# Optimization experiments

Hardware: AMD Instinct MI355X
Metric: run time of the kernel (lower is better)

The kernel has to match this reference:

```python
import jax, jax.numpy as jnp
import numpy as np

LAMBDA = 0.7
RATIO = 3
EPS = 1e-6


def setup_inputs() -> dict:
    key = jax.random.key(0)
    k1, k2, k3 = jax.random.split(key, 3)
    bs, n, w, h = 8, 7, 640, 640
    preds = jax.random.normal(k1, (bs, n, w, h), dtype=jnp.float32)
    labels = jax.random.randint(k2, (bs, n, w, h), 0, 2, dtype=jnp.int32)
    training_mask = jax.random.randint(k3, (bs, w, h), 0, 2, dtype=jnp.int32)
    return {"preds": preds, "labels": labels, "training_mask": training_mask}


def _dice(S, G):
    # S, G: [C, P]; per-channel dice coefficient, then mean over channels
    num = 2.0 * jnp.sum(S * G, axis=-1)
    den = jnp.sum(S * S, axis=-1) + jnp.sum(G * G, axis=-1) + EPS
    return jnp.mean(num / den)


def _single_sample(pred, label, mask):
    # pred, label: [n, P]; mask: [P]
    P = pred.shape[-1]
    p = jax.nn.sigmoid(pred)
    pred_n = p[-1] * mask            # masked full-text prediction
    label_n = label[-1] * mask

    # --- OHEM mask M (cal_M): keep all positives + top (ratio*n_pos) hardest negatives ---
    pos = pred_n >= 0.5
    n_pos = jnp.sum(pos)
    n_neg_all = jnp.sum(~pos)
    k = n_pos * RATIO
    # sigmoid outputs are in (0,1); sentinel -1 pushes positives to the end of the descending sort
    neg_vals = jnp.where(pos, -1.0, pred_n)
    sorted_desc = -jnp.sort(-neg_vals)
    thr = sorted_desc[jnp.clip(k - 1, 0, P - 1)]  # k-th largest negative score
    ohem_active = (n_neg_all > k) & (k > 0)
    M = jnp.where(ohem_active, (pred_n >= thr).astype(jnp.float32), 1.0)

    # L_c: dice loss on OHEM-selected full-text map
    L_c = 1.0 - _dice((pred_n * M)[None, :], (label_n * M)[None, :])

    # L_s: dice loss on shrunk kernels, gated by predicted text region W
    W = (pred_n >= 0.5).astype(jnp.float32)
    L_s = 1.0 - _dice(p[:-1] * W, label[:-1] * W)

    loss = LAMBDA * L_c + (1.0 - LAMBDA) * L_s
    return L_c, L_s, loss


def reference(preds, labels, training_mask):
    bs, n, w, h = preds.shape
    preds = preds.reshape(bs, n, w * h)
    labels = labels.reshape(bs, n, w * h).astype(jnp.float32)
    mask = training_mask.reshape(bs, w * h).astype(jnp.float32)
    L_c, L_s, loss = jax.vmap(_single_sample)(preds, labels, mask)
    # reduction='mean'
    return L_c.mean(), L_s.mean(), loss.mean()
```

## Files before the change

### kernel.cpp

```cpp
#include <hip/hip_runtime.h>

#define BS   8
#define NCH  7
#define PX   409600
#define NBIN 65536
#define NCHK 256
#define EPSF 1e-6f
#define NT   256
#define BPB  200

__device__ __forceinline__ float sigf(float x) {
    return 1.0f / (1.0f + __expf(-x));
}

__device__ __forceinline__ unsigned wred_u(unsigned v) {
    #pragma unroll
    for (int o = 32; o; o >>= 1) v += __shfl_down(v, o);
    return v;
}

__device__ __forceinline__ float wred_f(float v) {
    #pragma unroll
    for (int o = 32; o; o >>= 1) v += __shfl_down(v, o);
    return v;
}

__device__ void select2(const unsigned* __restrict__ chunks,
                        const unsigned* __restrict__ bins,
                        unsigned k, unsigned* out_bin, unsigned* out_rank) {
    __shared__ unsigned cs[256];
    int t = threadIdx.x;
    cs[t] = chunks[t];
    __syncthreads();
    #pragma unroll
    for (int off = 1; off < 256; off <<= 1) {
        unsigned v = cs[t];
        unsigned a = (t + off < 256) ? cs[t + off] : 0u;
        __syncthreads();
        cs[t] = v + a;
        __syncthreads();
    }
    {
        unsigned sfx  = cs[t];
        unsigned sfx1 = (t < 255) ? cs[t + 1] : 0u;
        if (sfx >= k && sfx1 < k) { *out_bin = (unsigned)t; *out_rank = k - sfx1; }
    }
    __syncthreads();
    unsigned chunk = *out_bin, krem = *out_rank;
    cs[t] = bins[chunk * 256 + t];
    __syncthreads();
    #pragma unroll
    for (int off = 1; off < 256; off <<= 1) {
        unsigned v = cs[t];
        unsigned a = (t + off < 256) ? cs[t + off] : 0u;
        __syncthreads();
        cs[t] = v + a;
        __syncthreads();
    }
    {
        unsigned sfx  = cs[t];
        unsigned sfx1 = (t < 255) ? cs[t + 1] : 0u;
        if (sfx >= krem && sfx1 < krem) {
            *out_bin  = chunk * 256 + (unsigned)t;
            *out_rank = krem - sfx1;
        }
    }
    __syncthreads();
}

__global__ __launch_bounds__(256) void k_main(
        const float* __restrict__ preds, const int* __restrict__ labels,
        const int* __restrict__ mask,
        float* __restrict__ psum,
        unsigned* __restrict__ ppos,
        unsigned* __restrict__ pzero,
        unsigned* __restrict__ done) {
    const int tid = threadIdx.x;
    const int b = blockIdx.y, cb = blockIdx.x;
    if (b == 0 && cb == 0 && tid == 0) *done = 0u;

    const float* pr = preds + (size_t)b * NCH * PX;
    const int*   lb = labels + (size_t)b * NCH * PX;
    const int*   mk = mask + (size_t)b * PX;

    float acc[21];
    #pragma unroll
    for (int j = 0; j < 21; j++) acc[j] = 0.f;
    unsigned cnt = 0;

    #pragma unroll
    for (int it = 0; it < 2; ++it) {
        const int g  = cb * NT + tid + it * (BPB * NT);
        const int px = g * 4;
        float4 p6 = *(const float4*)(pr + 6 * PX + px);
        int4   m4 = *(const int4*)(mk + px);
        int4   l6 = *(const int4*)(lb + 6 * PX + px);
        float4 pc[6];
        int4   lc[6];
        #pragma unroll
        for (int c = 0; c < 6; c++) pc[c] = *(const float4*)(pr + c * PX + px);
        #pragma unroll
        for (int c = 0; c < 6; c++) lc[c] = *(const int4*)(lb + c * PX + px);

        float mm[4]  = {(float)m4.x, (float)m4.y, (float)m4.z, (float)m4.w};
        float p6a[4] = {p6.x, p6.y, p6.z, p6.w};
        float l6a[4] = {(float)l6.x, (float)l6.y, (float)l6.z, (float)l6.w};
        float pn[4], W[4];
        #pragma unroll
        for (int u = 0; u < 4; u++) {
            pn[u] = sigf(p6a[u]) * mm[u];
            bool pos = (pn[u] >= 0.5f);
            W[u] = pos ? 1.0f : 0.0f;
            cnt += pos ? 1u : (__float_as_uint(pn[u]) == 0u ? 0x10000u : 0u);
        }
        #pragma unroll
        for (int c = 0; c < 6; c++) {
            float pcs[4] = {pc[c].x, pc[c].y, pc[c].z, pc[c].w};
            float lcs[4] = {(float)lc[c].x, (float)lc[c].y,
                            (float)lc[c].z, (float)lc[c].w};
            #pragma unroll
            for (int u = 0; u < 4; u++) {
                float s = sigf(pcs[u]);
                float l = lcs[u];
                acc[c]      += s * l * W[u];
                acc[6 + c]  += s * s * W[u];
                acc[12 + c] += l * W[u];
            }
        }
        #pragma unroll
        for (int u = 0; u < 4; u++) {
            float ln = l6a[u] * mm[u];
            acc[18] += pn[u] * ln;
            acc[19] += pn[u] * pn[u];
            acc[20] += ln;
        }
    }

    __shared__ float    red[4][21];
    __shared__ unsigned cred[4];
    int lane = tid & 63, wid = tid >> 6;
    #pragma unroll
    for (int j = 0; j < 21; j++) {
        float v = wred_f(acc[j]);
        if (lane == 0) red[wid][j] = v;
    }
    unsigned cv = wred_u(cnt);
    if (lane == 0) cred[wid] = cv;
    __syncthreads();
    if (tid < 21) {
        float tot = red[0][tid] + red[1][tid] + red[2][tid] + red[3][tid];
        psum[((size_t)b * 21 + tid) * BPB + cb] = tot;
    }
    if (tid == 21) {
        unsigned ct = cred[0] + cred[1] + cred[2] + cred[3];
        ppos[b * BPB + cb]  = ct & 0xFFFFu;
        pzero[b * BPB + cb] = ct >> 16;
    }
}

__global__ __launch_bounds__(256) void k_sel(
        const float* __restrict__ preds, const int* __restrict__ labels,
        const int* __restrict__ mask,
        const float* __restrict__ psum, const unsigned* __restrict__ ppos,
        const unsigned* __restrict__ pzero,
        unsigned* __restrict__ histws, unsigned* __restrict__ chunkws,
        float* __restrict__ lcls,
        unsigned* __restrict__ done, float* __restrict__ out) {
    const int tid = threadIdx.x;
    const int b = blockIdx.x;
    int lane = tid & 63, wid = tid >> 6;

    __shared__ unsigned uR[4][2];
    unsigned npv = (tid < BPB) ? ppos[b * BPB + tid] : 0u;
    unsigned zcv = (tid < BPB) ? pzero[b * BPB + tid] : 0u;
    unsigned r0 = wred_u(npv), r1 = wred_u(zcv);
    if (lane == 0) { uR[wid][0] = r0; uR[wid][1] = r1; }
    __syncthreads();
    const unsigned np = uR[0][0] + uR[1][0] + uR[2][0] + uR[3][0];
    const unsigned zc = uR[0][1] + uR[1][1] + uR[2][1] + uR[3][1];

    __shared__ float S[21];
    if (tid < 21) S[tid] = 0.f;
    __syncthreads();
    for (int i = tid; i < 21 * BPB; i += NT) {
        atomicAdd(&S[i / BPB], psum[(size_t)b * 21 * BPB + i]);
    }
    __syncthreads();

    const unsigned k = np * 3u;
    const bool active = ((unsigned)PX - np > k) && (k > 0u);
    const unsigned nzneg = (unsigned)PX - np - zc;

    float Lc_b;
    if (!active || k >= nzneg) {
        Lc_b = 1.0f - 2.0f * S[18] / (S[19] + S[20] + EPSF);
    } else {
        unsigned* h1 = histws + (size_t)b * NBIN;
        unsigned* c1 = chunkws + (size_t)b * NCHK;
        const float* pr6 = preds + ((size_t)b * NCH + 6) * PX;
        const int*   lb6 = labels + ((size_t)b * NCH + 6) * PX;
        const int*   mk  = mask + (size_t)b * PX;

        for (int j = tid; j < NBIN; j += NT) h1[j] = 0u;
        for (int j = tid; j < NCHK; j += NT) c1[j] = 0u;
        __syncthreads();
        for (int gg = tid; gg < PX; gg += NT) {
            float pnx = sigf(pr6[gg]) * (float)mk[gg];
            if (pnx < 0.5f) {
                unsigned bits = __float_as_uint(pnx);
                if (bits) {
                    atomicAdd(&h1[bits >> 16], 1u);
                    atomicAdd(&c1[bits >> 24], 1u);
                }
            }
        }
        __syncthreads();
        if (tid == 0) { atomicAdd(&h1[0], zc); atomicAdd(&c1[0], zc); }
        __syncthreads();

        __shared__ unsigned rb, rr, rb2, rr2;
        select2(c1, h1, k, &rb, &rr);
        float thrv;
        if (rb == 0u) {
            thrv = 0.0f;
        } else {
            unsigned hi = rb;
            for (int j = tid; j < NBIN; j += NT) h1[j] = 0u;
            for (int j = tid; j < NCHK; j += NT) c1[j] = 0u;
            __syncthreads();
            for (int gg = tid; gg < PX; gg += NT) {
                float pnx = sigf(pr6[gg]) * (float)mk[gg];
                if (pnx < 0.5f) {
                    unsigned bits = __float_as_uint(pnx);
                    if (bits && (bits >> 16) == hi) {
                        unsigned lo = bits & 0xFFFFu;
                        atomicAdd(&h1[lo], 1u);
                        atomicAdd(&c1[lo >> 8], 1u);
                    }
                }
            }
            __syncthreads();
            select2(c1, h1, rr, &rb2, &rr2);
            thrv = __uint_as_float((hi << 16) | rb2);
        }
        float a0 = 0.f, a1 = 0.f, a2 = 0.f;
        for (int gg = tid; gg < PX; gg += NT) {
            float m   = (float)mk[gg];
            float pnx = sigf(pr6[gg]) * m;
            if (pnx >= thrv) {
                float ln = (float)lb6[gg] * m;
                a0 += pnx * ln;
                a1 += pnx * pnx;
                a2 += ln;
            }
        }
        __shared__ float aR[4][3];
        float v0 = wred_f(a0), v1 = wred_f(a1), v2 = wred_f(a2);
        if (lane == 0) { aR[wid][0] = v0; aR[wid][1] = v1; aR[wid][2] = v2; }
        __syncthreads();
        float A0 = aR[0][0] + aR[1][0] + aR[2][0] + aR[3][0];
        float A1 = aR[0][1] + aR[1][1] + aR[2][1] + aR[3][1];
        float A2 = aR[0][2] + aR[1][2] + aR[2][2] + aR[3][2];
        Lc_b = 1.0f - 2.0f * A0 / (A1 + A2 + EPSF);
    }

    float ls_acc = 0.f;
    #pragma unroll
    for (int c = 0; c < 6; c++)
        ls_acc += (2.0f * S[c]) / (S[6 + c] + S[12 + c] + EPSF);
    float Ls_b = 1.0f - ls_acc * (1.0f / 6.0f);

    if (tid == 0) {
        lcls[b * 2]     = Lc_b;
        lcls[b * 2 + 1] = Ls_b;
    }

    __shared__ unsigned tick;
    if (tid == 0) {
        __threadfence();
        tick = atomicAdd(done, 1u);
    }
    __syncthreads();
    if (tick != (unsigned)(BS - 1)) return;
    __threadfence();

    float Lc = 0.f, Ls = 0.f;
    if (tid < BS) { Lc = lcls[tid * 2]; Ls = lcls[tid * 2 + 1]; }
    #pragma unroll
    for (int o = 4; o; o >>= 1) { Lc += __shfl_down(Lc, o); Ls += __shfl_down(Ls, o); }
    if (tid == 0) {
        float lc_m = Lc * (1.0f / (float)BS);
        float ls_m = Ls * (1.0f / (float)BS);
        out[0] = lc_m;
        out[1] = ls_m;
        out[2] = 0.7f * lc_m + 0.3f * ls_m;
    }
}

extern "C" void kernel_launch(void* const* d_in, const int* in_sizes, int n_in,
                              void* d_out, int out_size, void* d_ws, size_t ws_size,
                              hipStream_t stream) {
    const float* preds = (const float*)d_in[0];
    const int* labels  = (const int*)d_in[1];
    const int* mask    = (const int*)d_in[2];
    float* out = (float*)d_out;

    float*    psum    = (float*)d_ws;
    unsigned* ppos    = (unsigned*)(psum + BS * 21 * BPB);
    unsigned* pzero   = ppos + BS * BPB;
    unsigned* done    = pzero + BS * BPB;
    float*    lcls    = (float*)(done + 8);
    unsigned* histws  = (unsigned*)(lcls + BS * 2);
    unsigned* chunkws = histws + (size_t)BS * NBIN;
    (void)chunkws;

    hipLaunchKernelGGL(k_main, dim3(BPB, BS), dim3(NT), 0, stream,
                       preds, labels, mask, psum, ppos, pzero, done);

    hipLaunchKernelGGL(k_sel, dim3(BS), dim3(NT), 0, stream,
                       preds, labels, mask, psum, ppos, pzero,
                       histws, chunkws, lcls, done, out);
}
```

Baseline: 221.0 us.

## Split main pass into text-channel kernel and per-channel kernel using ballot masks

The single fused pass is replaced by two kernels. The first handles only the full-text channel: it computes the positive mask, writes it as per-wave ballot bitmasks and emits partial sums and counts. The second runs one block per (batch, channel, chunk), reads each channel's preds and labels plus the bitmask, and reduces dice terms. This is meant to raise parallelism and cut per-thread register pressure from the 21-accumulator loop. In exchange it adds an extra launch, a small bitmask round-trip through memory, and more partials for the select kernel to reduce.

Measured after the change: 224.3 us. About the same (+1.5%).

```diff
diff --git a/kernel.cpp b/kernel.cpp
--- a/kernel.cpp
+++ b/kernel.cpp
@@ -7,7 +7,8 @@
 #define NCHK 256
 #define EPSF 1e-6f
 #define NT   256
-#define BPB  200
+#define BPB  400
+#define NWAVE 1600
 
 __device__ __forceinline__ float sigf(float x) {
     return 1.0f / (1.0f + __expf(-x));
@@ -68,124 +69,158 @@
     __syncthreads();
 }
 
-__global__ __launch_bounds__(256) void k_main(
+__global__ __launch_bounds__(256) void k_a(
         const float* __restrict__ preds, const int* __restrict__ labels,
         const int* __restrict__ mask,
-        float* __restrict__ psum,
+        float* __restrict__ psumA,
         unsigned* __restrict__ ppos,
         unsigned* __restrict__ pzero,
+        unsigned long long* __restrict__ wm,
         unsigned* __restrict__ done) {
     const int tid = threadIdx.x;
     const int b = blockIdx.y, cb = blockIdx.x;
     if (b == 0 && cb == 0 && tid == 0) *done = 0u;
 
-    const float* pr = preds + (size_t)b * NCH * PX;
-    const int*   lb = labels + (size_t)b * NCH * PX;
-    const int*   mk = mask + (size_t)b * PX;
-
-    float acc[21];
-    #pragma unroll
-    for (int j = 0; j < 21; j++) acc[j] = 0.f;
-    unsigned cnt = 0;
-
-    #pragma unroll
-    for (int it = 0; it < 2; ++it) {
-        const int g  = cb * NT + tid + it * (BPB * NT);
-        const int px = g * 4;
-        float4 p6 = *(const float4*)(pr + 6 * PX + px);
-        int4   m4 = *(const int4*)(mk + px);
-        int4   l6 = *(const int4*)(lb + 6 * PX + px);
-        float4 pc[6];
-        int4   lc[6];
-        #pragma unroll
-        for (int c = 0; c < 6; c++) pc[c] = *(const float4*)(pr + c * PX + px);
-        #pragma unroll
-        for (int c = 0; c < 6; c++) lc[c] = *(const int4*)(lb + c * PX + px);
-
-        float mm[4]  = {(float)m4.x, (float)m4.y, (float)m4.z, (float)m4.w};
-        float p6a[4] = {p6.x, p6.y, p6.z, p6.w};
-        float l6a[4] = {(float)l6.x, (float)l6.y, (float)l6.z, (float)l6.w};
-        float pn[4], W[4];
-        #pragma unroll
-        for (int u = 0; u < 4; u++) {
-            pn[u] = sigf(p6a[u]) * mm[u];
-            bool pos = (pn[u] >= 0.5f);
-            W[u] = pos ? 1.0f : 0.0f;
-            cnt += pos ? 1u : (__float_as_uint(pn[u]) == 0u ? 0x10000u : 0u);
-        }
-        #pragma unroll
-        for (int c = 0; c < 6; c++) {
-            float pcs[4] = {pc[c].x, pc[c].y, pc[c].z, pc[c].w};
-            float lcs[4] = {(float)lc[c].x, (float)lc[c].y,
-                            (float)lc[c].z, (float)lc[c].w};
-            #pragma unroll
-            for (int u = 0; u < 4; u++) {
-                float s = sigf(pcs[u]);
-                float l = lcs[u];
-                acc[c]      += s * l * W[u];
-                acc[6 + c]  += s * s * W[u];
-                acc[12 + c] += l * W[u];
-            }
-        }
-        #pragma unroll
-        for (int u = 0; u < 4; u++) {
-            float ln = l6a[u] * mm[u];
-            acc[18] += pn[u] * ln;
-            acc[19] += pn[u] * pn[u];
-            acc[20] += ln;
-        }
-    }
-
-    __shared__ float    red[4][21];
-    __shared__ unsigned cred[4];
-    int lane = tid & 63, wid = tid >> 6;
-    #pragma unroll
-    for (int j = 0; j < 21; j++) {
-        float v = wred_f(acc[j]);
-        if (lane == 0) red[wid][j] = v;
-    }
-    unsigned cv = wred_u(cnt);
-    if (lane == 0) cred[wid] = cv;
-    __syncthreads();
-    if (tid < 21) {
+    const int g  = cb * NT + tid;
+    const int px = g * 4;
+    const float* pr6 = preds + ((size_t)b * NCH + 6) * PX;
+    const int*   lb6 = labels + ((size_t)b * NCH + 6) * PX;
+    const int*   mk  = mask + (size_t)b * PX;
+
+    float4 p6 = *(const float4*)(pr6 + px);
+    int4   l6 = *(const int4*)(lb6 + px);
+    int4   m4 = *(const int4*)(mk + px);
+
+    float mm[4]  = {(float)m4.x, (float)m4.y, (float)m4.z, (float)m4.w};
+    float p6a[4] = {p6.x, p6.y, p6.z, p6.w};
+    float l6a[4] = {(float)l6.x, (float)l6.y, (float)l6.z, (float)l6.w};
+
+    float pn[4];
+    unsigned long long bp[4], bz[4];
+    #pragma unroll
+    for (int u = 0; u < 4; u++) {
+        pn[u] = sigf(p6a[u]) * mm[u];
+        bp[u] = __ballot(pn[u] >= 0.5f);
+        bz[u] = __ballot(__float_as_uint(pn[u]) == 0u);
+    }
+
+    float a0 = 0.f, a1 = 0.f, a2 = 0.f;
+    #pragma unroll
+    for (int u = 0; u < 4; u++) {
+        float ln = l6a[u] * mm[u];
+        a0 += pn[u] * ln;
+        a1 += pn[u] * pn[u];
+        a2 += ln;
+    }
+
+    const int lane = tid & 63, wid = tid >> 6;
+    const int w = g >> 6;
+    if (lane == 0) {
+        ulonglong2* wp = (ulonglong2*)(wm + ((size_t)b * NWAVE + w) * 4);
+        wp[0] = make_ulonglong2(bp[0], bp[1]);
+        wp[1] = make_ulonglong2(bp[2], bp[3]);
+    }
+
+    __shared__ unsigned cpos[4], czer[4];
+    if (lane == 0) {
+        cpos[wid] = (unsigned)(__popcll(bp[0]) + __popcll(bp[1]) +
+                               __popcll(bp[2]) + __popcll(bp[3]));
+        czer[wid] = (unsigned)(__popcll(bz[0]) + __popcll(bz[1]) +
+                               __popcll(bz[2]) + __popcll(bz[3]));
+    }
+    __shared__ float red[4][3];
+    float v0 = wred_f(a0), v1 = wred_f(a1), v2 = wred_f(a2);
+    if (lane == 0) { red[wid][0] = v0; red[wid][1] = v1; red[wid][2] = v2; }
+    __syncthreads();
+    if (tid < 3) {
         float tot = red[0][tid] + red[1][tid] + red[2][tid] + red[3][tid];
-        psum[((size_t)b * 21 + tid) * BPB + cb] = tot;
-    }
-    if (tid == 21) {
-        unsigned ct = cred[0] + cred[1] + cred[2] + cred[3];
-        ppos[b * BPB + cb]  = ct & 0xFFFFu;
-        pzero[b * BPB + cb] = ct >> 16;
+        psumA[((size_t)b * 3 + tid) * BPB + cb] = tot;
+    }
+    if (tid == 3) ppos[b * BPB + cb]  = cpos[0] + cpos[1] + cpos[2] + cpos[3];
+    if (tid == 4) pzero[b * BPB + cb] = czer[0] + czer[1] + czer[2] + czer[3];
+}
+
+__global__ __launch_bounds__(256) void k_b(
+        const float* __restrict__ preds, const int* __restrict__ labels,
+        const unsigned long long* __restrict__ wm,
+        float* __restrict__ psumB) {
+    const int tid = threadIdx.x;
+    const int y = blockIdx.y;
+    const int b = y / 6, c = y % 6;
+    const int cb = blockIdx.x;
+    const int g  = cb * NT + tid;
+    const int px = g * 4;
+    const float* pc = preds + ((size_t)b * NCH + c) * PX;
+    const int*   lc = labels + ((size_t)b * NCH + c) * PX;
+
+    float4 p = *(const float4*)(pc + px);
+    int4   l = *(const int4*)(lc + px);
+    const int lane = tid & 63, wid = tid >> 6;
+    const int w = g >> 6;
+    const ulonglong2* wp = (const ulonglong2*)(wm + ((size_t)b * NWAVE + w) * 4);
+    ulonglong2 w01 = wp[0];
+    ulonglong2 w23 = wp[1];
+
+    float W[4] = { (float)((w01.x >> lane) & 1ull), (float)((w01.y >> lane) & 1ull),
+                   (float)((w23.x >> lane) & 1ull), (float)((w23.y >> lane) & 1ull) };
+    float pa[4] = {p.x, p.y, p.z, p.w};
+    float la[4] = {(float)l.x, (float)l.y, (float)l.z, (float)l.w};
+
+    float sn = 0.f, sp = 0.f, sl = 0.f;
+    #pragma unroll
+    for (int u = 0; u < 4; u++) {
+        float s  = sigf(pa[u]);
+        float lw = la[u] * W[u];
+        sn += s * lw;
+        sp += s * s * W[u];
+        sl += lw;
+    }
+
+    __shared__ float red[4][3];
+    float v0 = wred_f(sn), v1 = wred_f(sp), v2 = wred_f(sl);
+    if (lane == 0) { red[wid][0] = v0; red[wid][1] = v1; red[wid][2] = v2; }
+    __syncthreads();
+    if (tid < 3) {
+        float tot = red[0][tid] + red[1][tid] + red[2][tid] + red[3][tid];
+        psumB[((size_t)y * 3 + tid) * BPB + cb] = tot;
     }
 }
 
 __global__ __launch_bounds__(256) void k_sel(
         const float* __restrict__ preds, const int* __restrict__ labels,
         const int* __restrict__ mask,
-        const float* __restrict__ psum, const unsigned* __restrict__ ppos,
-        const unsigned* __restrict__ pzero,
+        const float* __restrict__ psumA, const float* __restrict__ psumB,
+        const unsigned* __restrict__ ppos, const unsigned* __restrict__ pzero,
         unsigned* __restrict__ histws, unsigned* __restrict__ chunkws,
-        float* __restrict__ lcls,
-        unsigned* __restrict__ done, float* __restrict__ out) {
+        float* __restrict__ lcls, unsigned* __restrict__ done,
+        float* __restrict__ out) {
     const int tid = threadIdx.x;
     const int b = blockIdx.x;
-    int lane = tid & 63, wid = tid >> 6;
-
-    __shared__ unsigned uR[4][2];
-    unsigned npv = (tid < BPB) ? ppos[b * BPB + tid] : 0u;
-    unsigned zcv = (tid < BPB) ? pzero[b * BPB + tid] : 0u;
-    unsigned r0 = wred_u(npv), r1 = wred_u(zcv);
-    if (lane == 0) { uR[wid][0] = r0; uR[wid][1] = r1; }
-    __syncthreads();
-    const unsigned np = uR[0][0] + uR[1][0] + uR[2][0] + uR[3][0];
-    const unsigned zc = uR[0][1] + uR[1][1] + uR[2][1] + uR[3][1];
+    const int lane = tid & 63, wid = tid >> 6;
 
     __shared__ float S[21];
+    __shared__ unsigned C[2];
     if (tid < 21) S[tid] = 0.f;
-    __syncthreads();
-    for (int i = tid; i < 21 * BPB; i += NT) {
-        atomicAdd(&S[i / BPB], psum[(size_t)b * 21 * BPB + i]);
-    }
-    __syncthreads();
+    if (tid < 2) C[tid] = 0u;
+    __syncthreads();
+    {
+        unsigned pc = 0, zc = 0;
+        for (int i = tid; i < BPB; i += NT) {
+            pc += ppos[b * BPB + i];
+            zc += pzero[b * BPB + i];
+        }
+        pc = wred_u(pc); zc = wred_u(zc);
+        if (lane == 0) { atomicAdd(&C[0], pc); atomicAdd(&C[1], zc); }
+    }
+    for (int i = tid; i < 3 * BPB; i += NT)
+        atomicAdd(&S[18 + i / BPB], psumA[(size_t)b * 3 * BPB + i]);
+    for (int i = tid; i < 18 * BPB; i += NT) {
+        int cch = i / (3 * BPB);
+        int j   = (i / BPB) % 3;
+        atomicAdd(&S[j * 6 + cch], psumB[(size_t)b * 18 * BPB + i]);
+    }
+    __syncthreads();
+    const unsigned np = C[0], zc = C[1];
 
     const unsigned k = np * 3u;
     const bool active = ((unsigned)PX - np > k) && (k > 0u);
@@ -305,19 +340,23 @@
     const int* mask    = (const int*)d_in[2];
     float* out = (float*)d_out;
 
-    float*    psum    = (float*)d_ws;
-    unsigned* ppos    = (unsigned*)(psum + BS * 21 * BPB);
-    unsigned* pzero   = ppos + BS * BPB;
-    unsigned* done    = pzero + BS * BPB;
-    float*    lcls    = (float*)(done + 8);
-    unsigned* histws  = (unsigned*)(lcls + BS * 2);
+    float*    psumA  = (float*)d_ws;
+    float*    psumB  = psumA + (size_t)BS * 3 * BPB;
+    unsigned* ppos   = (unsigned*)(psumB + (size_t)BS * 18 * BPB);
+    unsigned* pzero  = ppos + BS * BPB;
+    unsigned* done   = pzero + BS * BPB;
+    float*    lcls   = (float*)(done + 8);
+    unsigned long long* wm = (unsigned long long*)(lcls + BS * 2 + 2);
+    unsigned* histws = (unsigned*)(wm + (size_t)BS * NWAVE * 4);
     unsigned* chunkws = histws + (size_t)BS * NBIN;
-    (void)chunkws;
-
-    hipLaunchKernelGGL(k_main, dim3(BPB, BS), dim3(NT), 0, stream,
-                       preds, labels, mask, psum, ppos, pzero, done);
+
+    hipLaunchKernelGGL(k_a, dim3(BPB, BS), dim3(NT), 0, stream,
+                       preds, labels, mask, psumA, ppos, pzero, wm, done);
+
+    hipLaunchKernelGGL(k_b, dim3(BPB, BS * 6), dim3(NT), 0, stream,
+                       preds, labels, wm, psumB);
 
     hipLaunchKernelGGL(k_sel, dim3(BS), dim3(NT), 0, stream,
-                       preds, labels, mask, psum, ppos, pzero,
+                       preds, labels, mask, psumA, psumB, ppos, pzero,
                        histws, chunkws, lcls, done, out);
 }
```
